# Performance work log

Measured on AMD Instinct MI355X. Metric: run time of the kernel, lower is better.

## Reference

```python
import jax, jax.numpy as jnp
import numpy as np
from jax import lax

MARGIN = 0.2
NMAX = 1


def setup_inputs() -> dict:
    key = jax.random.key(0)
    k1, k2 = jax.random.split(key)
    N, D = 8192, 512
    imgs = jax.random.normal(k1, (N, D), dtype=jnp.float32)
    caps = jax.random.normal(k2, (N, D), dtype=jnp.float32)
    return {"imgs": imgs, "caps": caps}


def reference(imgs, caps):
    # scores[i, j] = <img_i, cap_j>  -> [N, N]
    scores = jnp.matmul(imgs, caps.T)
    diag = jnp.diagonal(scores)  # [N]
    s = scores - 2.0 * jnp.diag(diag)
    # top-nmax over columns (axis 0): hardest negative captions per caption slot
    max_c = lax.top_k(s.T, NMAX)[0].T  # [NMAX, N]
    # top-nmax over rows (axis 1): hardest negative images per image slot
    max_i = lax.top_k(s, NMAX)[0]      # [N, NMAX]
    neg_cap = jnp.sum(jnp.maximum(max_c + (MARGIN - diag)[None, :], 0.0))
    neg_img = jnp.sum(jnp.maximum(max_i + (MARGIN - diag)[:, None], 0.0))
    return neg_cap + neg_img
```

## Files before the change

kernel.cpp:

```cpp
#include <hip/hip_runtime.h>

#define N_ROWS 8192
#define DIM    512

typedef __attribute__((ext_vector_type(4))) float frag_cd;
typedef __attribute__((ext_vector_type(2))) long long v2ll;

__device__ __forceinline__ unsigned f2fp8(float x) {
    float a = fabsf(x);
    unsigned s = (__float_as_uint(x) >> 31) << 7;
    if (a < 0.015625f) return s;
    a = fminf(a, 448.f);
    unsigned u = __float_as_uint(a);
    u += 0x7FFFFu + ((u >> 20) & 1u);
    unsigned exp = (u >> 23) - 120u;
    unsigned mant = (u >> 20) & 7u;
    return s | (exp << 3) | mant;
}
__device__ __forceinline__ unsigned pack4fp8(float4 v) {
    return f2fp8(v.x) | (f2fp8(v.y) << 8) | (f2fp8(v.z) << 16) | (f2fp8(v.w) << 24);
}
__device__ __forceinline__ unsigned enc_f32(float f) {
    unsigned u = __float_as_uint(f);
    return (u & 0x80000000u) ? ~u : (u | 0x80000000u);
}
__device__ __forceinline__ float dec_f32(unsigned k) {
    return __uint_as_float((k & 0x80000000u) ? (k & 0x7FFFFFFFu) : ~k);
}


__global__ __launch_bounds__(256) void k_prep(const float* __restrict__ imgs,
                                              const float* __restrict__ caps,
                                              unsigned char* __restrict__ fimgs,
                                              unsigned char* __restrict__ fcaps,
                                              float* __restrict__ diag,
                                              unsigned* __restrict__ rowmax,
                                              unsigned* __restrict__ colmax) {
    const int cr = blockIdx.x;
    const int t  = threadIdx.x;
    const int rin = t & 15;
    const int g   = t >> 4;
    const int kp  = g >> 1;
    const int hc  = g & 1;
    const int row = cr * 16 + rin;
    const float* arow = imgs + (size_t)row * DIM;
    const float* brow = caps + (size_t)row * DIM;
    float dsum = 0.f;
    #pragma unroll
    for (int e = 0; e < 2; ++e) {
        const int cg = hc * 2 + e;
        const int c0 = kp * 64 + cg * 8;
        float4 a0 = *(const float4*)(arow + c0),      a1 = *(const float4*)(arow + c0 + 4);
        float4 a2 = *(const float4*)(arow + c0 + 32), a3 = *(const float4*)(arow + c0 + 36);
        float4 b0 = *(const float4*)(brow + c0),      b1 = *(const float4*)(brow + c0 + 4);
        float4 b2 = *(const float4*)(brow + c0 + 32), b3 = *(const float4*)(brow + c0 + 36);
        uint4 oa, ob;
        oa.x = pack4fp8(a0); oa.y = pack4fp8(a1); oa.z = pack4fp8(a2); oa.w = pack4fp8(a3);
        ob.x = pack4fp8(b0); ob.y = pack4fp8(b1); ob.z = pack4fp8(b2); ob.w = pack4fp8(b3);
        const size_t off = (size_t)cr * 8192 + kp * 1024 + (cg * 16 + rin) * 16;
        *(uint4*)(fimgs + off) = oa;
        *(uint4*)(fcaps + off) = ob;
        dsum += a0.x * b0.x + a0.y * b0.y + a0.z * b0.z + a0.w * b0.w
              + a1.x * b1.x + a1.y * b1.y + a1.z * b1.z + a1.w * b1.w
              + a2.x * b2.x + a2.y * b2.y + a2.z * b2.z + a2.w * b2.w
              + a3.x * b3.x + a3.y * b3.y + a3.z * b3.z + a3.w * b3.w;
    }
    __shared__ float sred[256];
    sred[t] = dsum;
    __syncthreads();
    if (t < 16) {
        float s = 0.f;
        #pragma unroll
        for (int k = 0; k < 16; ++k) s += sred[t + 16 * k];
        const int r = cr * 16 + t;
        diag[r] = s; rowmax[r] = 0u; colmax[r] = 0u;
    }
}

__global__ __launch_bounds__(256) void k_gemm(const unsigned char* __restrict__ A,
                                              const unsigned char* __restrict__ B,
                                              unsigned* __restrict__ rowmax,
                                              unsigned* __restrict__ colmax) {
    __shared__ unsigned char sA[2][8192];
    __shared__ unsigned char sB[2][8192];
    const int tid = threadIdx.x;
    const int w = tid >> 6, lane = tid & 63;
    const int i0 = (int)blockIdx.y << 7, j0 = (int)blockIdx.x << 7;
    const int q = lane >> 4, l15 = lane & 15;
    const int wrow = (w >> 1) << 6, wcol = (w & 1) << 6;

    const unsigned char* Ab = A + (size_t)(i0 >> 4) * 8192 + lane * 16;
    const unsigned char* Bb = B + (size_t)(j0 >> 4) * 8192 + lane * 16;

    frag_cd acc[4][4] = {};

    auto stage = [&](int bi, int kp) {
        #pragma unroll
        for (int j = 0; j < 2; ++j) {
            const int s = j * 4 + w;
            __builtin_amdgcn_global_load_lds(
                (const __attribute__((address_space(1))) unsigned int*)(Ab + (size_t)s * 8192 + kp * 1024),
                (__attribute__((address_space(3))) unsigned int*)(&sA[bi][(s << 10) + (lane << 4)]), 16, 0, 0);
            __builtin_amdgcn_global_load_lds(
                (const __attribute__((address_space(1))) unsigned int*)(Bb + (size_t)s * 8192 + kp * 1024),
                (__attribute__((address_space(3))) unsigned int*)(&sB[bi][(s << 10) + (lane << 4)]), 16, 0, 0);
        }
    };

    stage(0, 0);
    __syncthreads();

    const int u16 = ((q << 4) + l15) << 4;

    #pragma unroll
    for (int kp = 0; kp < 8; ++kp) {
        const int cur = kp & 1, nxt = cur ^ 1;
        if (kp < 7) stage(nxt, kp + 1);

        v2ll af[4], bfr[4];
        #pragma unroll
        for (int r = 0; r < 4; ++r)
            af[r] = *(const v2ll*)(&sA[cur][((((w >> 1) << 2) + r) << 10) + u16]);
        #pragma unroll
        for (int c = 0; c < 4; ++c)
            bfr[c] = *(const v2ll*)(&sB[cur][((((w & 1) << 2) + c) << 10) + u16]);
        #pragma unroll
        for (int r = 0; r < 4; ++r)
            #pragma unroll
            for (int c = 0; c < 4; ++c)
                acc[r][c] = __builtin_amdgcn_mfma_f32_16x16x32_fp8_fp8(af[r][0], bfr[c][0], acc[r][c], 0, 0, 0);
        #pragma unroll
        for (int r = 0; r < 4; ++r)
            #pragma unroll
            for (int c = 0; c < 4; ++c)
                acc[r][c] = __builtin_amdgcn_mfma_f32_16x16x32_fp8_fp8(af[r][1], bfr[c][1], acc[r][c], 0, 0, 0);

        __syncthreads();
    }

    const bool dblk = (i0 == j0);
    #pragma unroll
    for (int r = 0; r < 4; ++r)
        #pragma unroll
        for (int c = 0; c < 4; ++c)
            #pragma unroll
            for (int g = 0; g < 4; ++g) {
                float f = acc[r][c][g];
                if (dblk && (wrow + (r << 4) + (q << 2) + g) == (wcol + (c << 4) + l15))
                    f = -f;
                acc[r][c][g] = f;
            }

    #pragma unroll
    for (int r = 0; r < 4; ++r)
        #pragma unroll
        for (int g = 0; g < 4; ++g) {
            float m = fmaxf(fmaxf(acc[r][0][g], acc[r][1][g]),
                            fmaxf(acc[r][2][g], acc[r][3][g]));
            m = fmaxf(m, __shfl_xor(m, 1, 64));
            m = fmaxf(m, __shfl_xor(m, 2, 64));
            m = fmaxf(m, __shfl_xor(m, 4, 64));
            m = fmaxf(m, __shfl_xor(m, 8, 64));
            if (l15 == 0)
                atomicMax(&rowmax[i0 + wrow + (r << 4) + (q << 2) + g], enc_f32(m));
        }
    #pragma unroll
    for (int c = 0; c < 4; ++c) {
        float m = acc[0][c][0];
        #pragma unroll
        for (int r = 0; r < 4; ++r)
            #pragma unroll
            for (int g = 0; g < 4; ++g) m = fmaxf(m, acc[r][c][g]);
        m = fmaxf(m, __shfl_xor(m, 16, 64));
        m = fmaxf(m, __shfl_xor(m, 32, 64));
        if (q == 0)
            atomicMax(&colmax[j0 + wcol + (c << 4) + l15], enc_f32(m));
    }
}

__global__ __launch_bounds__(1024) void k_final(const unsigned* __restrict__ rowmax,
                                                const unsigned* __restrict__ colmax,
                                                const float* __restrict__ diag,
                                                float* __restrict__ out) {
    const int tid = threadIdx.x;
    float s = 0.f;
    #pragma unroll
    for (int i = 0; i < 8; ++i) {
        const int idx = tid + (i << 10);
        float d = diag[idx];
        s += fmaxf(dec_f32(rowmax[idx]) + 0.2f - d, 0.f);
        s += fmaxf(dec_f32(colmax[idx]) + 0.2f - d, 0.f);
    }
    #pragma unroll
    for (int m = 1; m < 64; m <<= 1) s += __shfl_xor(s, m, 64);
    __shared__ float red[16];
    if ((tid & 63) == 0) red[tid >> 6] = s;
    __syncthreads();
    if (tid == 0) {
        float t = 0.f;
        #pragma unroll
        for (int i = 0; i < 16; ++i) t += red[i];
        out[0] = t;
    }
}

extern "C" void kernel_launch(void* const* d_in, const int* in_sizes, int n_in,
                              void* d_out, int out_size, void* d_ws, size_t ws_size,
                              hipStream_t stream) {
    const float* imgs = (const float*)d_in[0];
    const float* caps = (const float*)d_in[1];
    float* out = (float*)d_out;

    char* ws = (char*)d_ws;
    unsigned char* fimgs = (unsigned char*)ws;
    unsigned char* fcaps = (unsigned char*)(ws + 4194304);
    float*    diag   = (float*)   (ws + 8388608);
    unsigned* rowmax = (unsigned*)(ws + 8388608 + 32768);
    unsigned* colmax = (unsigned*)(ws + 8388608 + 65536);

    k_prep<<<N_ROWS / 16, 256, 0, stream>>>(imgs, caps, fimgs, fcaps,
                                            diag, rowmax, colmax);
    k_gemm<<<dim3(64, 64), 256, 0, stream>>>(fimgs, fcaps, rowmax, colmax);
    k_final<<<1, 1024, 0, stream>>>(rowmax, colmax, diag, out);
}
```

Baseline: 173.5 us.

## Shrink GEMM tile to 64x128 with 4-block occupancy and rework fp8 prep layout

The GEMM block tile drops from 128x128 to 64x128, doubling the grid to 8192 blocks, halving per-warp accumulators, and adding a launch bound of four blocks per CU. The aim is more resident waves to hide latency and better load balance across CUs. The cost is more global fp8 traffic and roughly twice as many atomicMax reductions for rows and columns. The prep kernel is also restructured so each wave reads whole contiguous rows and reduces the diagonal dot product with wave shuffles instead of a shared-memory reduction.

After: 165.5 us. -4.6%, faster.

```diff
diff --git a/kernel.cpp b/kernel.cpp
--- a/kernel.cpp
+++ b/kernel.cpp
@@ -38,69 +38,61 @@
                                               unsigned* __restrict__ colmax) {
     const int cr = blockIdx.x;
     const int t  = threadIdx.x;
-    const int rin = t & 15;
-    const int g   = t >> 4;
-    const int kp  = g >> 1;
-    const int hc  = g & 1;
-    const int row = cr * 16 + rin;
-    const float* arow = imgs + (size_t)row * DIM;
-    const float* brow = caps + (size_t)row * DIM;
-    float dsum = 0.f;
-    #pragma unroll
-    for (int e = 0; e < 2; ++e) {
-        const int cg = hc * 2 + e;
-        const int c0 = kp * 64 + cg * 8;
-        float4 a0 = *(const float4*)(arow + c0),      a1 = *(const float4*)(arow + c0 + 4);
-        float4 a2 = *(const float4*)(arow + c0 + 32), a3 = *(const float4*)(arow + c0 + 36);
-        float4 b0 = *(const float4*)(brow + c0),      b1 = *(const float4*)(brow + c0 + 4);
-        float4 b2 = *(const float4*)(brow + c0 + 32), b3 = *(const float4*)(brow + c0 + 36);
-        uint4 oa, ob;
-        oa.x = pack4fp8(a0); oa.y = pack4fp8(a1); oa.z = pack4fp8(a2); oa.w = pack4fp8(a3);
-        ob.x = pack4fp8(b0); ob.y = pack4fp8(b1); ob.z = pack4fp8(b2); ob.w = pack4fp8(b3);
-        const size_t off = (size_t)cr * 8192 + kp * 1024 + (cg * 16 + rin) * 16;
-        *(uint4*)(fimgs + off) = oa;
-        *(uint4*)(fcaps + off) = ob;
-        dsum += a0.x * b0.x + a0.y * b0.y + a0.z * b0.z + a0.w * b0.w
-              + a1.x * b1.x + a1.y * b1.y + a1.z * b1.z + a1.w * b1.w
-              + a2.x * b2.x + a2.y * b2.y + a2.z * b2.z + a2.w * b2.w
-              + a3.x * b3.x + a3.y * b3.y + a3.z * b3.z + a3.w * b3.w;
-    }
-    __shared__ float sred[256];
-    sred[t] = dsum;
-    __syncthreads();
-    if (t < 16) {
-        float s = 0.f;
-        #pragma unroll
-        for (int k = 0; k < 16; ++k) s += sred[t + 16 * k];
-        const int r = cr * 16 + t;
-        diag[r] = s; rowmax[r] = 0u; colmax[r] = 0u;
-    }
-}
-
-__global__ __launch_bounds__(256) void k_gemm(const unsigned char* __restrict__ A,
-                                              const unsigned char* __restrict__ B,
-                                              unsigned* __restrict__ rowmax,
-                                              unsigned* __restrict__ colmax) {
-    __shared__ unsigned char sA[2][8192];
+    const int w = t >> 6, l = t & 63;
+    const int kp = l >> 3, cg = l & 3, par = (l >> 2) & 1;
+    const size_t ubase = (size_t)cr * 8192 + kp * 1024 + cg * 256 + par * 8;
+    float ps[4];
+    #pragma unroll
+    for (int i = 0; i < 4; ++i) {
+        const int row = w + 4 * i;
+        const float* ar = imgs + ((size_t)cr * 16 + row) * DIM + l * 8;
+        const float* br = caps + ((size_t)cr * 16 + row) * DIM + l * 8;
+        float4 a0 = *(const float4*)ar, a1 = *(const float4*)(ar + 4);
+        float4 b0 = *(const float4*)br, b1 = *(const float4*)(br + 4);
+        uint2 oa, ob;
+        oa.x = pack4fp8(a0); oa.y = pack4fp8(a1);
+        ob.x = pack4fp8(b0); ob.y = pack4fp8(b1);
+        *(uint2*)(fimgs + ubase + row * 16) = oa;
+        *(uint2*)(fcaps + ubase + row * 16) = ob;
+        ps[i] = a0.x * b0.x + a0.y * b0.y + a0.z * b0.z + a0.w * b0.w
+              + a1.x * b1.x + a1.y * b1.y + a1.z * b1.z + a1.w * b1.w;
+    }
+    #pragma unroll
+    for (int i = 0; i < 4; ++i) {
+        float s = ps[i];
+        #pragma unroll
+        for (int m = 1; m < 64; m <<= 1) s += __shfl_xor(s, m, 64);
+        if (l == 0) {
+            const int r = cr * 16 + w + 4 * i;
+            diag[r] = s; rowmax[r] = 0u; colmax[r] = 0u;
+        }
+    }
+}
+
+__global__ __launch_bounds__(256, 4) void k_gemm(const unsigned char* __restrict__ A,
+                                                 const unsigned char* __restrict__ B,
+                                                 unsigned* __restrict__ rowmax,
+                                                 unsigned* __restrict__ colmax) {
+    __shared__ unsigned char sA[2][4096];
     __shared__ unsigned char sB[2][8192];
     const int tid = threadIdx.x;
     const int w = tid >> 6, lane = tid & 63;
-    const int i0 = (int)blockIdx.y << 7, j0 = (int)blockIdx.x << 7;
+    const int j0 = (int)blockIdx.x << 7, i0 = (int)blockIdx.y << 6;
     const int q = lane >> 4, l15 = lane & 15;
-    const int wrow = (w >> 1) << 6, wcol = (w & 1) << 6;
+    const int wr = (w & 1) << 5, wc = (w >> 1) << 6;
 
     const unsigned char* Ab = A + (size_t)(i0 >> 4) * 8192 + lane * 16;
     const unsigned char* Bb = B + (size_t)(j0 >> 4) * 8192 + lane * 16;
 
-    frag_cd acc[4][4] = {};
+    frag_cd acc[2][4] = {};
 
     auto stage = [&](int bi, int kp) {
+        __builtin_amdgcn_global_load_lds(
+            (const __attribute__((address_space(1))) unsigned int*)(Ab + (size_t)w * 8192 + kp * 1024),
+            (__attribute__((address_space(3))) unsigned int*)(&sA[bi][(w << 10) + (lane << 4)]), 16, 0, 0);
         #pragma unroll
         for (int j = 0; j < 2; ++j) {
-            const int s = j * 4 + w;
-            __builtin_amdgcn_global_load_lds(
-                (const __attribute__((address_space(1))) unsigned int*)(Ab + (size_t)s * 8192 + kp * 1024),
-                (__attribute__((address_space(3))) unsigned int*)(&sA[bi][(s << 10) + (lane << 4)]), 16, 0, 0);
+            const int s = 2 * w + j;
             __builtin_amdgcn_global_load_lds(
                 (const __attribute__((address_space(1))) unsigned int*)(Bb + (size_t)s * 8192 + kp * 1024),
                 (__attribute__((address_space(3))) unsigned int*)(&sB[bi][(s << 10) + (lane << 4)]), 16, 0, 0);
@@ -117,20 +109,20 @@
         const int cur = kp & 1, nxt = cur ^ 1;
         if (kp < 7) stage(nxt, kp + 1);
 
-        v2ll af[4], bfr[4];
-        #pragma unroll
-        for (int r = 0; r < 4; ++r)
-            af[r] = *(const v2ll*)(&sA[cur][((((w >> 1) << 2) + r) << 10) + u16]);
+        v2ll af[2], bfr[4];
+        #pragma unroll
+        for (int r = 0; r < 2; ++r)
+            af[r] = *(const v2ll*)(&sA[cur][((((w & 1) << 1) + r) << 10) + u16]);
         #pragma unroll
         for (int c = 0; c < 4; ++c)
-            bfr[c] = *(const v2ll*)(&sB[cur][((((w & 1) << 2) + c) << 10) + u16]);
-        #pragma unroll
-        for (int r = 0; r < 4; ++r)
+            bfr[c] = *(const v2ll*)(&sB[cur][((((w >> 1) << 2) + c) << 10) + u16]);
+        #pragma unroll
+        for (int r = 0; r < 2; ++r)
             #pragma unroll
             for (int c = 0; c < 4; ++c)
                 acc[r][c] = __builtin_amdgcn_mfma_f32_16x16x32_fp8_fp8(af[r][0], bfr[c][0], acc[r][c], 0, 0, 0);
         #pragma unroll
-        for (int r = 0; r < 4; ++r)
+        for (int r = 0; r < 2; ++r)
             #pragma unroll
             for (int c = 0; c < 4; ++c)
                 acc[r][c] = __builtin_amdgcn_mfma_f32_16x16x32_fp8_fp8(af[r][1], bfr[c][1], acc[r][c], 0, 0, 0);
@@ -138,21 +130,22 @@
         __syncthreads();
     }
 
-    const bool dblk = (i0 == j0);
-    #pragma unroll
-    for (int r = 0; r < 4; ++r)
+    const bool dblk = ((i0 >> 7) == (int)blockIdx.x);
+    #pragma unroll
+    for (int r = 0; r < 2; ++r)
         #pragma unroll
         for (int c = 0; c < 4; ++c)
             #pragma unroll
             for (int g = 0; g < 4; ++g) {
                 float f = acc[r][c][g];
-                if (dblk && (wrow + (r << 4) + (q << 2) + g) == (wcol + (c << 4) + l15))
-                    f = -f;
+                const int gi = wr + (r << 4) + (q << 2) + g;
+                const int gj = wc + (c << 4) + l15;
+                if (dblk && (i0 + gi) == (j0 + gj)) f = -f;
                 acc[r][c][g] = f;
             }
 
     #pragma unroll
-    for (int r = 0; r < 4; ++r)
+    for (int r = 0; r < 2; ++r)
         #pragma unroll
         for (int g = 0; g < 4; ++g) {
             float m = fmaxf(fmaxf(acc[r][0][g], acc[r][1][g]),
@@ -162,19 +155,19 @@
             m = fmaxf(m, __shfl_xor(m, 4, 64));
             m = fmaxf(m, __shfl_xor(m, 8, 64));
             if (l15 == 0)
-                atomicMax(&rowmax[i0 + wrow + (r << 4) + (q << 2) + g], enc_f32(m));
+                atomicMax(&rowmax[i0 + wr + (r << 4) + (q << 2) + g], enc_f32(m));
         }
     #pragma unroll
     for (int c = 0; c < 4; ++c) {
         float m = acc[0][c][0];
         #pragma unroll
-        for (int r = 0; r < 4; ++r)
+        for (int r = 0; r < 2; ++r)
             #pragma unroll
             for (int g = 0; g < 4; ++g) m = fmaxf(m, acc[r][c][g]);
         m = fmaxf(m, __shfl_xor(m, 16, 64));
         m = fmaxf(m, __shfl_xor(m, 32, 64));
         if (q == 0)
-            atomicMax(&colmax[j0 + wcol + (c << 4) + l15], enc_f32(m));
+            atomicMax(&colmax[j0 + wc + (c << 4) + l15], enc_f32(m));
     }
 }
 
@@ -220,6 +213,6 @@
 
     k_prep<<<N_ROWS / 16, 256, 0, stream>>>(imgs, caps, fimgs, fcaps,
                                             diag, rowmax, colmax);
-    k_gemm<<<dim3(64, 64), 256, 0, stream>>>(fimgs, fcaps, rowmax, colmax);
+    k_gemm<<<dim3(64, 128), 256, 0, stream>>>(fimgs, fcaps, rowmax, colmax);
     k_final<<<1, 1024, 0, stream>>>(rowmax, colmax, diag, out);
 }
```
